# Performance work log

Measured on AMD Instinct MI355X. Metric: run time of the kernel, lower is better.

Reference implementation:

```python
import jax, jax.numpy as jnp
import numpy as np
import math

N_HEADS = 16
D_HEAD = 64
D_MODEL = 1024
ROPE_THETA = 10000.0


def setup_inputs() -> dict:
    key = jax.random.key(0)
    k1, k2, k3 = jax.random.split(key, 3)
    B, T = 2, 2048
    x = jax.random.normal(k1, (B, T, D_MODEL), dtype=jnp.float32)
    # torch Linear(in, out) weight has shape (out, in); store transposed (in, out)
    # so forward is x @ w. Scale like default init to keep activations sane.
    w_qkv = jax.random.normal(k2, (D_MODEL, 3 * D_MODEL), dtype=jnp.float32) / math.sqrt(D_MODEL)
    w_o = jax.random.normal(k3, (D_MODEL, D_MODEL), dtype=jnp.float32) / math.sqrt(D_MODEL)
    return {"x": x, "w_qkv": w_qkv, "w_o": w_o}


def _build_rope(T, dtype):
    inv_freq = 1.0 / (ROPE_THETA ** (jnp.arange(0, D_HEAD, 2, dtype=jnp.float32) / D_HEAD))
    t = jnp.arange(T, dtype=jnp.float32)
    freqs = jnp.outer(t, inv_freq)            # [T, D_HEAD/2]
    emb = jnp.concatenate([freqs, freqs], -1)  # [T, D_HEAD]
    return jnp.cos(emb).astype(dtype), jnp.sin(emb).astype(dtype)


def _apply_rope(x, cos, sin):
    # x: [B, T, H, D_HEAD]; cos/sin broadcast as [1, T, 1, D_HEAD]
    x1, x2 = jnp.split(x, 2, axis=-1)
    rotated = jnp.concatenate([-x2, x1], axis=-1)
    return x * cos + rotated * sin


def reference(x, w_qkv, w_o):
    B, T, D = x.shape
    qkv = (x @ w_qkv).reshape(B, T, 3, N_HEADS, D_HEAD)
    q, k, v = qkv[:, :, 0], qkv[:, :, 1], qkv[:, :, 2]  # [B, T, H, Dh]
    cos, sin = _build_rope(T, x.dtype)
    cos = cos[None, :, None, :]
    sin = sin[None, :, None, :]
    q = _apply_rope(q, cos, sin)
    k = _apply_rope(k, cos, sin)
    scale = 1.0 / math.sqrt(D_HEAD)
    # full [B, H, T, T] scores (faithful to the manual matmul-softmax-matmul)
    attn = jnp.einsum("bthd,bshd->bhts", q, k) * scale
    attn = jax.nn.softmax(attn, axis=-1)
    out = jnp.einsum("bhts,bshd->bthd", attn, v).reshape(B, T, D)
    return out @ w_o
```

## Files before the change

kernel.cpp:

```cpp
#include <hip/hip_runtime.h>
#include <cstdint>

typedef unsigned short ushort_t;
typedef __attribute__((ext_vector_type(8))) short v8s;
typedef __attribute__((ext_vector_type(4))) short v4s;
typedef __attribute__((ext_vector_type(2))) unsigned v2u;
typedef __attribute__((ext_vector_type(4))) float v4f;

#define MFMA(a, b, c) __builtin_amdgcn_mfma_f32_16x16x32_bf16(a, b, c, 0, 0, 0)
#define QSCALE 0.18033688011112042f

#define GLL(gp, lp) __builtin_amdgcn_global_load_lds(                        \
    (const __attribute__((address_space(1))) void*)(gp),                     \
    (__attribute__((address_space(3))) void*)(lp), 16, 0, 0)

#define WAIT_LGKM0() __builtin_amdgcn_s_waitcnt(0xc07f)

__device__ __forceinline__ float bf2f(ushort_t u) {
    union { unsigned u; float f; } x; x.u = ((unsigned)u) << 16; return x.f;
}
__device__ __forceinline__ short f2bf(float f) {
    union { float f; unsigned u; } x; x.f = f;
    unsigned r = x.u + 0x7fffu + ((x.u >> 16) & 1u);
    return (short)(r >> 16);
}

__global__ __launch_bounds__(256) void prep(const void* __restrict__ xin,
                                            const void* __restrict__ w1,
                                            const void* __restrict__ w2,
                                            ushort_t* __restrict__ xb,
                                            ushort_t* __restrict__ out1,
                                            ushort_t* __restrict__ out2,
                                            int* __restrict__ flag,
                                            float* __restrict__ tab) {
    __shared__ ushort_t tile[64][65];
    __shared__ int cnt;
    int bid = blockIdx.x, tid = threadIdx.x;

    int isbf = 0;
    if (bid < 3072 || bid == 3328) {
        if (tid == 0) cnt = 0;
        __syncthreads();
        unsigned w = ((const unsigned*)xin)[tid];
        int e = (w >> 7) & 0xFF;
        int hit = ((e >= 96 && e <= 135) || (w & 0xFFFFu) == 0) ? 1 : 0;
        atomicAdd(&cnt, hit);
        __syncthreads();
        isbf = (cnt >= 160) ? 1 : 0;
        if (bid == 3328) {
            if (tid == 0) *flag = isbf;
            return;
        }
    }

    if (bid < 2048) {
        int i = bid * 256 + tid;
        if (isbf) {
            ((v8s*)xb)[i] = ((const v8s*)xin)[i];
        } else {
            const float* xf = (const float*)xin + (size_t)i * 8;
            v8s o;
            #pragma unroll
            for (int j = 0; j < 8; ++j) o[j] = f2bf(xf[j]);
            ((v8s*)xb)[i] = o;
        }
    } else if (bid < 3072) {
        int t = bid - 2048;
        int bxl = t & 63, by = (t >> 6) * 64;
        const void* in; ushort_t* out; int C, bx;
        if (bxl < 48) { in = w1; out = out1; C = 3072; bx = bxl * 64; }
        else          { in = w2; out = out2; C = 1024; bx = (bxl - 48) * 64; }
        const int R = 1024;
        int tx = tid & 63, ty = tid >> 6;
        for (int i = ty; i < 64; i += 4) {
            size_t idx = (size_t)(by + i) * C + bx + tx;
            tile[i][tx] = isbf ? ((const ushort_t*)in)[idx]
                               : (ushort_t)f2bf(((const float*)in)[idx]);
        }
        __syncthreads();
        for (int i = ty; i < 64; i += 4) out[(size_t)(bx + i) * R + by + tx] = tile[tx][i];
    } else {
        int idx = (bid - 3072) * 256 + tid;
        int d = idx >> 11, t = idx & 2047;
        float inv_freq = __expf(-(float)d * 0.28782313662425575f);
        float ang = (float)t * inv_freq;
        float sn, cs;
        sincosf(ang, &sn, &cs);
        tab[d * 2048 + t]         = bf2f((ushort_t)f2bf(cs));
        tab[65536 + d * 2048 + t] = bf2f((ushort_t)f2bf(sn));
    }
}

template <int MODE, int BN>
__global__ __launch_bounds__(256) void gemm_bt(const ushort_t* __restrict__ A,
                                               const ushort_t* __restrict__ BT,
                                               void* __restrict__ C,
                                               const int* __restrict__ flagp,
                                               int M, int N, int K,
                                               ushort_t* __restrict__ Qp,
                                               ushort_t* __restrict__ Kp,
                                               ushort_t* __restrict__ Vp,
                                               const float* __restrict__ tab) {
    constexpr int NJ = BN / 32;
    __shared__ __align__(16) ushort_t As[2][128 * 32];
    __shared__ __align__(16) ushort_t Bs[2][BN * 32];
    int tid = threadIdx.x;
    int lane = tid & 63;
    int lr = lane & 15, lc = lane >> 4;
    int w = tid >> 6;
    int wr = (w >> 1) * 64, wc = (w & 1) * (BN / 2);

    int nx = gridDim.x;
    int orig = blockIdx.y * nx + blockIdx.x;
    int cpx = (nx * gridDim.y) >> 3;
    int swz = (orig & 7) * cpx + (orig >> 3);
    int m0 = (swz / nx) * 128, n0 = (swz % nx) * BN;

    int c0 = tid, c1 = tid + 256;
    int r0 = c0 >> 2, s0 = c0 & 3;
    int r1 = c1 >> 2, s1 = c1 & 3;

    const ushort_t* Ag0 = A + (size_t)(m0 + r0) * K + s0 * 8;
    const ushort_t* Ag1 = A + (size_t)(m0 + r1) * K + s1 * 8;
    const ushort_t* Bg0 = BT + (size_t)(n0 + r0) * K + s0 * 8;
    const ushort_t* Bg1 = BT + (size_t)(n0 + r1) * K + s1 * 8;
    const int aoff0 = w * 512;
    const int aoff1 = 2048 + w * 512;
    const int boff0 = w * 512;
    const int boff1 = 2048 + w * 512;

    v4f acc[4][NJ] = {};

    GLL(Ag0, &As[0][aoff0]);
    GLL(Ag1, &As[0][aoff1]);
    GLL(Bg0, &Bs[0][boff0]);
    if constexpr (BN == 128) GLL(Bg1, &Bs[0][boff1]);
    __syncthreads();

    int buf = 0;
    for (int kt = 0; kt < K; kt += 32) {
        if (kt + 32 < K) {
            int nb = buf ^ 1;
            GLL(Ag0 + kt + 32, &As[nb][aoff0]);
            GLL(Ag1 + kt + 32, &As[nb][aoff1]);
            GLL(Bg0 + kt + 32, &Bs[nb][boff0]);
            if constexpr (BN == 128) GLL(Bg1 + kt + 32, &Bs[nb][boff1]);
        }

        v8s af[4], bfr[NJ];
        #pragma unroll
        for (int i = 0; i < 4; ++i)
            af[i] = *(const v8s*)(&As[buf][0] + (wr + i * 16 + lr) * 32 + lc * 8);
        #pragma unroll
        for (int j = 0; j < NJ; ++j)
            bfr[j] = *(const v8s*)(&Bs[buf][0] + (wc + j * 16 + lr) * 32 + lc * 8);
        #pragma unroll
        for (int i = 0; i < 4; ++i)
            #pragma unroll
            for (int j = 0; j < NJ; ++j)
                acc[i][j] = MFMA(af[i], bfr[j], acc[i][j]);

        __syncthreads();
        buf ^= 1;
    }

    if (MODE == 1) {
        int store_f32 = (*flagp == 0);
        #pragma unroll
        for (int i = 0; i < 4; ++i)
            #pragma unroll
            for (int j = 0; j < NJ; ++j)
                #pragma unroll
                for (int r = 0; r < 4; ++r) {
                    int row = m0 + wr + i * 16 + lc * 4 + r;
                    int col = n0 + wc + j * 16 + lr;
                    if (store_f32)
                        ((float*)C)[(size_t)row * N + col] = acc[i][j][r];
                    else
                        ((ushort_t*)C)[(size_t)row * N + col] = (ushort_t)f2bf(acc[i][j][r]);
                }
    } else {
        int region = n0 >> 10;
        int h = ((n0 & 1023) + wc) >> 6;
        if (region < 2) {
            const float sc = (region == 0) ? QSCALE : 1.0f;
            ushort_t* dst = (region == 0) ? Qp : Kp;
            #pragma unroll
            for (int i = 0; i < 4; ++i)
                #pragma unroll
                for (int j = 0; j < 2; ++j) {
                    int d = j * 16 + lr;
                    int tg0 = m0 + wr + i * 16 + lc * 4;
                    int b = tg0 >> 11, tt0 = tg0 & 2047;
                    v4f cs4 = *(const v4f*)(tab + d * 2048 + tt0);
                    v4f sn4 = *(const v4f*)(tab + 65536 + d * 2048 + tt0);
                    #pragma unroll
                    for (int r = 0; r < 4; ++r) {
                        float x1 = acc[i][j][r], x2 = acc[i][(j + 2) % NJ][r];
                        size_t base = ((size_t)(b * 16 + h) * 2048 + tt0 + r) * 64 + d;
                        dst[base]      = (ushort_t)f2bf((x1 * cs4[r] - x2 * sn4[r]) * sc);
                        dst[base + 32] = (ushort_t)f2bf((x2 * cs4[r] + x1 * sn4[r]) * sc);
                    }
                }
        } else {
            #pragma unroll
            for (int i = 0; i < 4; ++i)
                #pragma unroll
                for (int j = 0; j < NJ; ++j) {
                    int d = j * 16 + lr;
                    int tg0 = m0 + wr + i * 16 + lc * 4;
                    int b = tg0 >> 11, tt = tg0 & 2047;
                    v4s pk;
                    #pragma unroll
                    for (int r = 0; r < 4; ++r) pk[r] = f2bf(acc[i][j][r]);
                    size_t base = (size_t)(b * 16 + h) * 131072 + (size_t)(tt >> 5) * 2048
                                + (size_t)d * 32 + (tt & 31);
                    *(v4s*)(Vp + base) = pk;
                }
        }
    }
}

__global__ __launch_bounds__(256, 4) void gemm_o(const ushort_t* __restrict__ A,
                                                 const ushort_t* __restrict__ BT,
                                                 void* __restrict__ C,
                                                 const int* __restrict__ flagp) {
    constexpr int K = 1024, N = 1024;
    __shared__ __align__(16) ushort_t As[2][64 * 64];
    __shared__ __align__(16) ushort_t Bs[2][64 * 64];
    int tid = threadIdx.x;
    int lane = tid & 63;
    int lr = lane & 15, lc = lane >> 4;
    int w = tid >> 6;
    int wr = (w >> 1) * 32, wc = (w & 1) * 32;

    int nx = gridDim.x;
    int orig = blockIdx.y * nx + blockIdx.x;
    int cpx = (nx * gridDim.y) >> 3;
    int swz = (orig & 7) * cpx + (orig >> 3);
    int m0 = (swz / nx) * 64, n0 = (swz % nx) * 64;

    const ushort_t* ag[2]; const ushort_t* bg[2];
    int lof[2];
    #pragma unroll
    for (int q = 0; q < 2; ++q) {
        int c = q * 256 + tid, r = c >> 3, p = c & 7;
        ag[q] = A + (size_t)(m0 + r) * K + ((p ^ (r & 7)) * 8);
        bg[q] = BT + (size_t)(n0 + r) * K + ((p ^ (r & 7)) * 8);
        lof[q] = (q * 256 + w * 64) * 8;
    }

    v4f acc[2][2] = {};

    #pragma unroll
    for (int q = 0; q < 2; ++q) GLL(ag[q], &As[0][lof[q]]);
    #pragma unroll
    for (int q = 0; q < 2; ++q) GLL(bg[q], &Bs[0][lof[q]]);
    __syncthreads();

    int buf = 0;
    for (int t = 0; t < 16; ++t) {
        if (t + 1 < 16) {
            int kg = (t + 1) * 64, nb = buf ^ 1;
            #pragma unroll
            for (int q = 0; q < 2; ++q) GLL(ag[q] + kg, &As[nb][lof[q]]);
            #pragma unroll
            for (int q = 0; q < 2; ++q) GLL(bg[q] + kg, &Bs[nb][lof[q]]);
        }

        v8s af[2][2], bf[2][2];
        #pragma unroll
        for (int i = 0; i < 2; ++i)
            #pragma unroll
            for (int kk = 0; kk < 2; ++kk)
                af[i][kk] = *(const v8s*)(&As[buf][0] + (wr + i * 16 + lr) * 64
                                          + (((kk * 4 + lc) ^ (lr & 7)) * 8));
        #pragma unroll
        for (int j = 0; j < 2; ++j)
            #pragma unroll
            for (int kk = 0; kk < 2; ++kk)
                bf[j][kk] = *(const v8s*)(&Bs[buf][0] + (wc + j * 16 + lr) * 64
                                          + (((kk * 4 + lc) ^ (lr & 7)) * 8));
        __builtin_amdgcn_s_setprio(1);
        #pragma unroll
        for (int i = 0; i < 2; ++i)
            #pragma unroll
            for (int j = 0; j < 2; ++j) {
                acc[i][j] = MFMA(af[i][0], bf[j][0], acc[i][j]);
                acc[i][j] = MFMA(af[i][1], bf[j][1], acc[i][j]);
            }
        __builtin_amdgcn_s_setprio(0);

        __syncthreads();
        buf ^= 1;
    }

    int store_f32 = (*flagp == 0);
    #pragma unroll
    for (int i = 0; i < 2; ++i)
        #pragma unroll
        for (int j = 0; j < 2; ++j)
            #pragma unroll
            for (int r = 0; r < 4; ++r) {
                int row = m0 + wr + i * 16 + lc * 4 + r;
                int col = n0 + wc + j * 16 + lr;
                if (store_f32)
                    ((float*)C)[(size_t)row * N + col] = acc[i][j][r];
                else
                    ((ushort_t*)C)[(size_t)row * N + col] = (ushort_t)f2bf(acc[i][j][r]);
            }
}

__global__ __launch_bounds__(512) void attn(const ushort_t* __restrict__ Qr,
                                            const ushort_t* __restrict__ Kr,
                                            const ushort_t* __restrict__ Vt,
                                            ushort_t* __restrict__ AO) {
    __shared__ __align__(16) char lds[53248];
    int tid = threadIdx.x, lane = tid & 63, W = tid >> 6;
    int lr = lane & 15, lc = lane >> 4;
    int qsub = W & 1, sh = W >> 1;
    int L = blockIdx.x;
    int bh = (L & 7) * 4 + ((L >> 3) & 3);
    int qt = L >> 5;
    int q0 = qt * 128 + qsub * 64;
    int b = bh >> 4, h = bh & 15;
    const ushort_t* Qb = Qr + ((size_t)bh * 2048 + q0) * 64;
    const ushort_t* Kb = Kr + (size_t)bh * 131072 + (size_t)sh * 32768;
    const ushort_t* Vb = Vt + (size_t)bh * 131072 + (size_t)sh * 32768;
    ushort_t* KsG = (ushort_t*)(lds + sh * 8192);

    int gt = tid & 127;
    int c0 = gt, c1 = gt + 128;
    int kr0 = c0 >> 3, kc0 = c0 & 7, kr1 = c1 >> 3, kc1 = c1 & 7;
    const ushort_t* Kg0 = Kb + (size_t)kr0 * 64 + kc0 * 8;
    const ushort_t* Kg1 = Kb + (size_t)kr1 * 64 + kc1 * 8;
    int kl0 = kr0 * 64 + (kc0 ^ (kr0 & 7)) * 8;
    int kl1 = kr1 * 64 + (kc1 ^ (kr1 & 7)) * 8;

    int blr = (lr >> 2) * 8 + (lr & 3);

    v8s qf[4][2];
    #pragma unroll
    for (int jq = 0; jq < 4; ++jq)
        #pragma unroll
        for (int kk = 0; kk < 2; ++kk)
            qf[jq][kk] = *(const v8s*)(Qb + (size_t)(jq * 16 + lr) * 64 + kk * 32 + lc * 8);

    v4f o[4][4] = {};
    float li[4] = {0.f, 0.f, 0.f, 0.f};

    v8s ka = *(const v8s*)(Kg0), kb2 = *(const v8s*)(Kg1);
    *(v8s*)(KsG + kl0) = ka;
    *(v8s*)(KsG + kl1) = kb2;
    ka  = *(const v8s*)(Kg0 + 2048);
    kb2 = *(const v8s*)(Kg1 + 2048);
    __syncthreads();

    #pragma unroll 1
    for (int t = 0; t < 16; ++t) {
        int p = t & 1;
        const ushort_t* Kl = KsG + p * 2048;
        const ushort_t* Vg = Vb + (size_t)t * 2048;

        v8s vf[4];
        #pragma unroll
        for (int i = 0; i < 4; ++i)
            vf[i] = *(const v8s*)(Vg + (i * 16 + lr) * 32 + lc * 8);

        v8s kf[2][2];
        #pragma unroll
        for (int hh = 0; hh < 2; ++hh) {
            int rn = blr + hh * 4;
            int sw = hh * 4 + (lr & 3);
            #pragma unroll
            for (int kk = 0; kk < 2; ++kk)
                kf[hh][kk] = *(const v8s*)(Kl + rn * 64 + (((kk * 4 + lc) ^ sw) * 8));
        }

        v4f St[2][4] = {};
        __builtin_amdgcn_s_setprio(1);
        #pragma unroll
        for (int hh = 0; hh < 2; ++hh)
            #pragma unroll
            for (int jq = 0; jq < 4; ++jq) {
                St[hh][jq] = MFMA(kf[hh][0], qf[jq][0], St[hh][jq]);
                St[hh][jq] = MFMA(kf[hh][1], qf[jq][1], St[hh][jq]);
            }
        __builtin_amdgcn_s_setprio(0);

        if (t + 1 < 16) {
            ushort_t* Kn = KsG + (p ^ 1) * 2048;
            *(v8s*)(Kn + kl0) = ka;
            *(v8s*)(Kn + kl1) = kb2;
        }
        if (t + 2 < 16) {
            ka  = *(const v8s*)(Kg0 + (size_t)(t + 2) * 2048);
            kb2 = *(const v8s*)(Kg1 + (size_t)(t + 2) * 2048);
        }

        v8s pf[4];
        #pragma unroll
        for (int jq = 0; jq < 4; ++jq) {
            union { unsigned u[4]; v8s v; } P;
            #pragma unroll
            for (int hh = 0; hh < 2; ++hh) {
                #pragma unroll
                for (int r = 0; r < 4; ++r) {
                    float ev = __builtin_amdgcn_exp2f(St[hh][jq][r]);
                    St[hh][jq][r] = ev;
                    li[jq] += ev;
                }
                P.u[hh * 2 + 0] = __builtin_amdgcn_perm(__float_as_uint(St[hh][jq][1]),
                                                        __float_as_uint(St[hh][jq][0]), 0x07060302u);
                P.u[hh * 2 + 1] = __builtin_amdgcn_perm(__float_as_uint(St[hh][jq][3]),
                                                        __float_as_uint(St[hh][jq][2]), 0x07060302u);
            }
            pf[jq] = P.v;
        }
        __builtin_amdgcn_s_setprio(1);
        #pragma unroll
        for (int jq = 0; jq < 4; ++jq)
            #pragma unroll
            for (int i = 0; i < 4; ++i)
                o[i][jq] = MFMA(vf[i], pf[jq], o[i][jq]);
        __builtin_amdgcn_s_setprio(0);
        WAIT_LGKM0();
        __builtin_amdgcn_s_barrier();
    }

    #pragma unroll
    for (int jq = 0; jq < 4; ++jq) {
        li[jq] += __shfl_xor(li[jq], 16);
        li[jq] += __shfl_xor(li[jq], 32);
    }

    float* MO = (float*)lds;
    float* Ml = (float*)(lds + 52224);
    __syncthreads();
    #pragma unroll 1
    for (int ph = 0; ph < 2; ++ph) {
        if (qsub == ph && sh != 0) {
            float* M = MO + (sh - 1) * 4352;
            #pragma unroll
            for (int jq = 0; jq < 4; ++jq) {
                #pragma unroll
                for (int i = 0; i < 4; ++i)
                    *(v4f*)(M + (jq * 16 + lr) * 68 + i * 16 + lc * 4) = o[i][jq];
                if (lc == 0) Ml[(sh - 1) * 64 + jq * 16 + lr] = li[jq];
            }
        }
        __syncthreads();
        if (qsub == ph && sh == 0) {
            #pragma unroll
            for (int jq = 0; jq < 4; ++jq) {
                int row = jq * 16 + lr;
                float ls = li[jq] + Ml[row] + Ml[64 + row] + Ml[128 + row];
                float inv = 1.0f / ls;
                int tq = q0 + row;
                #pragma unroll
                for (int i = 0; i < 4; ++i) {
                    v4f m0v = *(const v4f*)(MO + row * 68 + i * 16 + lc * 4);
                    v4f m1v = *(const v4f*)(MO + 4352 + row * 68 + i * 16 + lc * 4);
                    v4f m2v = *(const v4f*)(MO + 8704 + row * 68 + i * 16 + lc * 4);
                    v4s pk;
                    #pragma unroll
                    for (int r = 0; r < 4; ++r)
                        pk[r] = f2bf((o[i][jq][r] + m0v[r] + m1v[r] + m2v[r]) * inv);
                    *(v4s*)(AO + (size_t)(b * 2048 + tq) * 1024 + h * 64 + i * 16 + lc * 4) = pk;
                }
            }
        }
        __syncthreads();
    }
}

extern "C" void kernel_launch(void* const* d_in, const int* in_sizes, int n_in,
                              void* d_out, int out_size, void* d_ws, size_t ws_size,
                              hipStream_t stream) {
    char* ws = (char*)d_ws;
    int*      flag  = (int*)ws;
    ushort_t* wqkvT = (ushort_t*)(ws + 256);
    ushort_t* woT   = (ushort_t*)(ws + 6291712);
    ushort_t* xb    = (ushort_t*)(ws + 8388864);
    ushort_t* Qr    = (ushort_t*)(ws + 16777472);
    ushort_t* Kr    = (ushort_t*)(ws + 25166080);
    ushort_t* Vt    = (ushort_t*)(ws + 33554688);
    ushort_t* AO    = (ushort_t*)(ws + 41943296);
    float*    tab   = (float*)(ws + 50331904);

    prep<<<3329, 256, 0, stream>>>(d_in[0], d_in[1], d_in[2], xb, wqkvT, woT, flag, tab);
    gemm_bt<2, 128><<<dim3(24, 32), 256, 0, stream>>>(xb, wqkvT, nullptr, flag, 4096, 3072, 1024,
                                                      Qr, Kr, Vt, tab);
    attn<<<512, 512, 0, stream>>>(Qr, Kr, Vt, AO);
    gemm_o<<<dim3(16, 64), 256, 0, stream>>>(AO, woT, d_out, flag);
}
```

Baseline: 186.6 us.

## Give each wave a private K tile in LDS to drop per-iteration barriers

```diff
diff --git a/kernel.cpp b/kernel.cpp
--- a/kernel.cpp
+++ b/kernel.cpp
@@ -315,7 +315,7 @@
                                             const ushort_t* __restrict__ Kr,
                                             const ushort_t* __restrict__ Vt,
                                             ushort_t* __restrict__ AO) {
-    __shared__ __align__(16) char lds[53248];
+    __shared__ __align__(16) char lds[65536];
     int tid = threadIdx.x, lane = tid & 63, W = tid >> 6;
     int lr = lane & 15, lc = lane >> 4;
     int qsub = W & 1, sh = W >> 1;
@@ -327,15 +327,16 @@
     const ushort_t* Qb = Qr + ((size_t)bh * 2048 + q0) * 64;
     const ushort_t* Kb = Kr + (size_t)bh * 131072 + (size_t)sh * 32768;
     const ushort_t* Vb = Vt + (size_t)bh * 131072 + (size_t)sh * 32768;
-    ushort_t* KsG = (ushort_t*)(lds + sh * 8192);
-
-    int gt = tid & 127;
-    int c0 = gt, c1 = gt + 128;
-    int kr0 = c0 >> 3, kc0 = c0 & 7, kr1 = c1 >> 3, kc1 = c1 & 7;
-    const ushort_t* Kg0 = Kb + (size_t)kr0 * 64 + kc0 * 8;
-    const ushort_t* Kg1 = Kb + (size_t)kr1 * 64 + kc1 * 8;
-    int kl0 = kr0 * 64 + (kc0 ^ (kr0 & 7)) * 8;
-    int kl1 = kr1 * 64 + (kc1 ^ (kr1 & 7)) * 8;
+    ushort_t* KsW = (ushort_t*)(lds + W * 8192);
+
+    const ushort_t* Kg[4];
+    int kl[4];
+    #pragma unroll
+    for (int q = 0; q < 4; ++q) {
+        int c = q * 64 + lane, r = c >> 3, pcol = c & 7;
+        Kg[q] = Kb + (size_t)r * 64 + pcol * 8;
+        kl[q] = r * 64 + (pcol ^ (r & 7)) * 8;
+    }
 
     int blr = (lr >> 2) * 8 + (lr & 3);
 
@@ -349,17 +350,18 @@
     v4f o[4][4] = {};
     float li[4] = {0.f, 0.f, 0.f, 0.f};
 
-    v8s ka = *(const v8s*)(Kg0), kb2 = *(const v8s*)(Kg1);
-    *(v8s*)(KsG + kl0) = ka;
-    *(v8s*)(KsG + kl1) = kb2;
-    ka  = *(const v8s*)(Kg0 + 2048);
-    kb2 = *(const v8s*)(Kg1 + 2048);
-    __syncthreads();
+    v8s kp[4];
+    #pragma unroll
+    for (int q = 0; q < 4; ++q) kp[q] = *(const v8s*)(Kg[q]);
+    #pragma unroll
+    for (int q = 0; q < 4; ++q) *(v8s*)(KsW + kl[q]) = kp[q];
+    #pragma unroll
+    for (int q = 0; q < 4; ++q) kp[q] = *(const v8s*)(Kg[q] + 2048);
 
     #pragma unroll 1
     for (int t = 0; t < 16; ++t) {
         int p = t & 1;
-        const ushort_t* Kl = KsG + p * 2048;
+        const ushort_t* Kl = KsW + p * 2048;
         const ushort_t* Vg = Vb + (size_t)t * 2048;
 
         v8s vf[4];
@@ -389,13 +391,13 @@
         __builtin_amdgcn_s_setprio(0);
 
         if (t + 1 < 16) {
-            ushort_t* Kn = KsG + (p ^ 1) * 2048;
-            *(v8s*)(Kn + kl0) = ka;
-            *(v8s*)(Kn + kl1) = kb2;
+            ushort_t* Kn = KsW + (p ^ 1) * 2048;
+            #pragma unroll
+            for (int q = 0; q < 4; ++q) *(v8s*)(Kn + kl[q]) = kp[q];
         }
         if (t + 2 < 16) {
-            ka  = *(const v8s*)(Kg0 + (size_t)(t + 2) * 2048);
-            kb2 = *(const v8s*)(Kg1 + (size_t)(t + 2) * 2048);
+            #pragma unroll
+            for (int q = 0; q < 4; ++q) kp[q] = *(const v8s*)(Kg[q] + (size_t)(t + 2) * 2048);
         }
 
         v8s pf[4];
@@ -424,8 +426,6 @@
             for (int i = 0; i < 4; ++i)
                 o[i][jq] = MFMA(vf[i], pf[jq], o[i][jq]);
         __builtin_amdgcn_s_setprio(0);
-        WAIT_LGKM0();
-        __builtin_amdgcn_s_barrier();
     }
 
     #pragma unroll
```

After: 188.9 us. No clear change (+1.2%).
